# Performance work log

Hardware: AMD Instinct MI355X
Metric: run time of the kernel (lower is better)

Reference implementation:

```python
import jax, jax.numpy as jnp
import numpy as np

D_MODEL = 1024
NHEAD = 16
HEAD_DIM = D_MODEL // NHEAD
B, T = 2, 2048


def setup_inputs() -> dict:
    key = jax.random.key(0)
    ks = jax.random.split(key, 12)
    s = 1.0 / np.sqrt(D_MODEL)
    return {
        "query": jax.random.normal(ks[0], (B, T, D_MODEL), jnp.float32),
        "key": jax.random.normal(ks[1], (B, T, D_MODEL), jnp.float32),
        "value": jax.random.normal(ks[2], (B, T, D_MODEL), jnp.float32),
        "key_padding_mask": jnp.zeros((B, T), dtype=bool),
        "attn_mask": jnp.zeros((T, T), jnp.float32),
        "stoich_frac": jax.random.uniform(ks[3], (B, T), jnp.float32),
        "Wq": jax.random.uniform(ks[4], (D_MODEL, D_MODEL), jnp.float32, -s, s),
        "bq": jnp.zeros((D_MODEL,), jnp.float32),
        "Wk": jax.random.uniform(ks[5], (D_MODEL, D_MODEL), jnp.float32, -s, s),
        "bk": jnp.zeros((D_MODEL,), jnp.float32),
        "Wv": jax.random.uniform(ks[6], (D_MODEL, D_MODEL), jnp.float32, -s, s),
        "bv": jnp.zeros((D_MODEL,), jnp.float32),
        "Wo": jax.random.uniform(ks[7], (D_MODEL, D_MODEL), jnp.float32, -s, s),
        "bo": jnp.zeros((D_MODEL,), jnp.float32),
        "stoich_alpha": jnp.float32(0.1),
    }


def reference(query, key, value, key_padding_mask, attn_mask, stoich_frac,
              Wq, bq, Wk, bk, Wv, bv, Wo, bo, stoich_alpha):
    Bq, Tq, _ = query.shape
    Tk = key.shape[1]
    scale = HEAD_DIM ** -0.5
    # Linear projections (torch Linear: x @ W.T + b), reshape to [B, H, T, Dh]
    Q = (query @ Wq.T + bq).reshape(Bq, Tq, NHEAD, HEAD_DIM).transpose(0, 2, 1, 3)
    K = (key @ Wk.T + bk).reshape(Bq, Tk, NHEAD, HEAD_DIM).transpose(0, 2, 1, 3)
    V = (value @ Wv.T + bv).reshape(Bq, Tk, NHEAD, HEAD_DIM).transpose(0, 2, 1, 3)
    # Scores [B, H, Tq, Tk]
    scores = jnp.einsum("bhqd,bhkd->bhqk", Q, K) * scale
    # Stoichiometric pairwise bias (T_q == T_k path)
    diff = stoich_frac[:, :, None] - stoich_frac[:, None, :]  # [B, Tq, Tk]
    bias = stoich_alpha * (jnp.log1p(jnp.abs(diff)) * jnp.sign(diff))
    scores = scores + bias[:, None, :, :]
    scores = scores + attn_mask  # broadcasts [Tq, Tk]
    scores = jnp.where(key_padding_mask[:, None, None, :], -jnp.inf, scores)
    probs = jax.nn.softmax(scores, axis=-1)
    # dropout: eval mode / p=0 -> identity
    out = jnp.einsum("bhqk,bhkd->bhqd", probs, V)
    out = out.transpose(0, 2, 1, 3).reshape(Bq, Tq, D_MODEL)
    return out @ Wo.T + bo
```

## Files before the change

### kernel.cpp

```cpp
#include <hip/hip_runtime.h>
#include <math.h>

typedef __bf16 bf16_t;
typedef __bf16 bf16x8 __attribute__((ext_vector_type(8)));
typedef __bf16 bf16x4 __attribute__((ext_vector_type(4)));
typedef float  f32x4  __attribute__((ext_vector_type(4)));

#define NHEAD 16
#define HDIM 64
#define DMODEL 1024
#define TSEQ 2048
#define WEL (DMODEL * DMODEL)

#define SBAR() __builtin_amdgcn_s_barrier()
#define SCHED0() __builtin_amdgcn_sched_barrier(0)
#define LGKM0() do { asm volatile("s_waitcnt lgkmcnt(0)" ::: "memory"); \
                     __builtin_amdgcn_sched_barrier(0); } while (0)

__device__ __forceinline__ f32x4 mfma16(bf16x8 a, bf16x8 b, f32x4 c) {
  return __builtin_amdgcn_mfma_f32_16x16x32_bf16(a, b, c, 0, 0, 0);
}

__device__ __forceinline__ void gload16(const bf16_t* g, bf16_t* l) {
  __builtin_amdgcn_global_load_lds((const __attribute__((address_space(1))) void*)g,
                                   (__attribute__((address_space(3))) void*)l, 16, 0, 0);
}

__device__ __forceinline__ unsigned pk2(float lo, float hi) {
  unsigned short a = __builtin_bit_cast(unsigned short, (__bf16)lo);
  unsigned short c = __builtin_bit_cast(unsigned short, (__bf16)hi);
  return ((unsigned)c << 16) | a;
}

__device__ __forceinline__ void cvtstore(f32x4 x0, f32x4 x1, bf16_t* dh, bf16_t* dl, int off) {
  bf16x8 hfr, lfr;
#pragma unroll
  for (int j = 0; j < 4; ++j) {
    float v = x0[j];
    __bf16 hb = (__bf16)v;
    hfr[j] = hb; lfr[j] = (__bf16)(v - (float)hb);
    float w = x1[j];
    __bf16 wb = (__bf16)w;
    hfr[4 + j] = wb; lfr[4 + j] = (__bf16)(w - (float)wb);
  }
  *(bf16x8*)(dh + off) = hfr;
  *(bf16x8*)(dl + off) = lfr;
}

__global__ __launch_bounds__(256)
void presplit_w(const float* __restrict__ w0, const float* __restrict__ w1,
                const float* __restrict__ w2, const float* __restrict__ w3,
                bf16_t* __restrict__ out) {
  const int y = blockIdx.y;
  const float* src = (y == 0) ? w0 : (y == 1) ? w1 : (y == 2) ? w2 : w3;
  size_t i = ((size_t)blockIdx.x * 256 + threadIdx.x) * 8;
  f32x4 a = *(const f32x4*)(src + i);
  f32x4 c = *(const f32x4*)(src + i + 4);
  bf16x8 h, l;
#pragma unroll
  for (int j = 0; j < 4; ++j) {
    __bf16 hb = (__bf16)a[j];
    h[j] = hb; l[j] = (__bf16)(a[j] - (float)hb);
    __bf16 cb = (__bf16)c[j];
    h[4 + j] = cb; l[4 + j] = (__bf16)(c[j] - (float)cb);
  }
  bf16_t* dh = out + (size_t)y * 2 * WEL;
  *(bf16x8*)(dh + i) = h;
  *(bf16x8*)(dh + WEL + i) = l;
}

__global__ __launch_bounds__(256)
void build_bias(const float* __restrict__ amask, const unsigned char* __restrict__ kpm,
                const float* __restrict__ sf, const float* __restrict__ alpha_p,
                bf16_t* __restrict__ BM) {
  size_t idx = (size_t)blockIdx.x * 256 + threadIdx.x;
  int k8 = (int)(idx & (TSEQ / 8 - 1));
  size_t bq = idx >> 8;
  int b = (int)(bq >> 11);
  int q = (int)(bq & (TSEQ - 1));
  const float sfq = sf[bq];
  const float alpha = *alpha_p;
  const float* sfk = sf + (size_t)b * TSEQ + k8 * 8;
  const float* am  = amask + (size_t)q * TSEQ + k8 * 8;
  const unsigned char* kp = kpm + (size_t)b * TSEQ + k8 * 8;
  bf16x8 o;
#pragma unroll
  for (int j = 0; j < 8; ++j) {
    float df = sfq - sfk[j];
    float v = alpha * copysignf(log1pf(fabsf(df)), df) + am[j];
    if (kp[j]) v = -1.0e30f;
    o[j] = (__bf16)v;
  }
  *(bf16x8*)&BM[idx * 8] = o;
}

template<int MODE>
__global__ __launch_bounds__(512)
void gemm_qkv(const float* __restrict__ A, const bf16_t* __restrict__ Wh,
              const bf16_t* __restrict__ Wl, const float* __restrict__ bias,
              bf16_t* __restrict__ obh, bf16_t* __restrict__ obl) {
  __shared__ bf16_t AH[8 * 512], AL[8 * 512], WHs[2][4 * 512], WLs[2][4 * 512];
  const int tid = threadIdx.x;
  const int lane = tid & 63;
  const int a15 = lane & 15, g = lane >> 4;
  const int wv = tid >> 6, wm = wv >> 1, wn = wv & 1;
  const int m0 = blockIdx.y * 128, n0 = blockIdx.x * 64;
  f32x4 acc[2][2] = {};

  const int t0 = tid >> 6, l0 = tid & 63;
  const float* pA = A + (size_t)(m0 + t0 * 16 + (l0 & 15)) * DMODEL + 8 * (l0 >> 4);
  const int wts = wv & 3;
  const bf16_t* pWg = ((wv < 4) ? Wh : Wl) + (size_t)(n0 + wts * 16 + a15) * DMODEL + 8 * g;

  f32x4 rAa = *(const f32x4*)pA, rAb = *(const f32x4*)(pA + 4);
  gload16(pWg, (wv < 4) ? &WHs[0][wts * 512] : &WLs[0][wts * 512]);

  constexpr int NK = DMODEL / 32;
  for (int t = 0; t < NK; ++t) {
    const int cur = t & 1;
    SBAR();
    cvtstore(rAa, rAb, AH, AL, tid * 8);
    SCHED0();
    if (t + 1 < NK) {
      pA += 32;
      rAa = *(const f32x4*)pA; rAb = *(const f32x4*)(pA + 4);
      SCHED0();
      gload16(pWg + (t + 1) * 32, (wv < 4) ? &WHs[cur ^ 1][wts * 512]
                                           : &WLs[cur ^ 1][wts * 512]);
      SCHED0();
      asm volatile("s_waitcnt vmcnt(3)" ::: "memory");
    } else {
      asm volatile("s_waitcnt vmcnt(0)" ::: "memory");
    }
    LGKM0();
    SBAR();

    bf16x8 ah[2], al[2], wh[2], wl[2];
#pragma unroll
    for (int i = 0; i < 2; ++i) {
      ah[i] = *(const bf16x8*)&AH[(wm * 2 + i) * 512 + lane * 8];
      al[i] = *(const bf16x8*)&AL[(wm * 2 + i) * 512 + lane * 8];
      wh[i] = *(const bf16x8*)&WHs[cur][(wn * 2 + i) * 512 + lane * 8];
      wl[i] = *(const bf16x8*)&WLs[cur][(wn * 2 + i) * 512 + lane * 8];
    }
    __builtin_amdgcn_s_setprio(1);
    if (MODE == 2) {
#pragma unroll
      for (int i = 0; i < 2; ++i)
#pragma unroll
        for (int j = 0; j < 2; ++j) {
          acc[i][j] = mfma16(wh[i], ah[j], acc[i][j]);
          acc[i][j] = mfma16(wh[i], al[j], acc[i][j]);
          acc[i][j] = mfma16(wl[i], ah[j], acc[i][j]);
        }
    } else {
#pragma unroll
      for (int i = 0; i < 2; ++i)
#pragma unroll
        for (int j = 0; j < 2; ++j) {
          acc[i][j] = mfma16(ah[i], wh[j], acc[i][j]);
          acc[i][j] = mfma16(ah[i], wl[j], acc[i][j]);
          acc[i][j] = mfma16(al[i], wh[j], acc[i][j]);
        }
    }
    __builtin_amdgcn_s_setprio(0);
  }

  if (MODE == 1) {
#pragma unroll
    for (int i = 0; i < 2; ++i)
#pragma unroll
      for (int j = 0; j < 2; ++j) {
        int n = n0 + wn * 32 + j * 16 + a15;
        float bs = bias[n];
        int hh = n >> 6, d = n & 63;
#pragma unroll
        for (int r = 0; r < 4; ++r) {
          int m = m0 + wm * 32 + i * 16 + 4 * g + r;
          int bb = m >> 11, t = m & (TSEQ - 1);
          float v = acc[i][j][r] + bs;
          size_t o = (((size_t)(bb * NHEAD + hh)) * TSEQ + t) * HDIM + d;
          __bf16 hb = (__bf16)v;
          obh[o] = hb;
          obl[o] = (__bf16)(v - (float)hb);
        }
      }
  } else {
#pragma unroll
    for (int i = 0; i < 2; ++i)
#pragma unroll
      for (int j = 0; j < 2; ++j) {
        int m = m0 + wm * 32 + j * 16 + a15;
        int bb = m >> 11, t = m & (TSEQ - 1);
#pragma unroll
        for (int r = 0; r < 4; ++r) {
          int n = n0 + wn * 32 + i * 16 + 4 * g + r;
          float v = acc[i][j][r] + bias[n];
          int hh = n >> 6, d = n & 63;
          size_t o = (((size_t)(bb * NHEAD + hh)) * HDIM + d) * TSEQ + t;
          __bf16 hb = (__bf16)v;
          obh[o] = hb;
          obl[o] = (__bf16)(v - (float)hb);
        }
      }
  }
}

__global__ __launch_bounds__(512)
void gemm_out(const bf16_t* __restrict__ Ah, const bf16_t* __restrict__ Al,
              const bf16_t* __restrict__ Wh, const bf16_t* __restrict__ Wl,
              const float* __restrict__ bias, float* __restrict__ of) {
  __shared__ bf16_t AHs[2][8 * 512], ALs[2][8 * 512], WHs[2][4 * 512], WLs[2][4 * 512];
  const int tid = threadIdx.x;
  const int lane = tid & 63;
  const int a15 = lane & 15, g = lane >> 4;
  const int wv = tid >> 6, wm = wv >> 1, wn = wv & 1;
  const int m0 = blockIdx.y * 128, n0 = blockIdx.x * 64;
  f32x4 acc[2][2] = {};

  const bf16_t* pAh = Ah + (size_t)(m0 + wv * 16 + a15) * DMODEL + 8 * g;
  const bf16_t* pAl = Al + (size_t)(m0 + wv * 16 + a15) * DMODEL + 8 * g;
  const int wts = wv & 3;
  const bf16_t* pWg = ((wv < 4) ? Wh : Wl) + (size_t)(n0 + wts * 16 + a15) * DMODEL + 8 * g;

  auto stage = [&](int t, int buf) {
    gload16(pAh + t * 32, &AHs[buf][wv * 512]);
    gload16(pAl + t * 32, &ALs[buf][wv * 512]);
    gload16(pWg + t * 32, (wv < 4) ? &WHs[buf][wts * 512] : &WLs[buf][wts * 512]);
  };
  stage(0, 0);

  constexpr int NK = DMODEL / 32;
  for (int t = 0; t < NK; ++t) {
    const int cur = t & 1;
    if (t + 1 < NK) {
      stage(t + 1, cur ^ 1);
      asm volatile("s_waitcnt vmcnt(3)" ::: "memory");
    } else {
      asm volatile("s_waitcnt vmcnt(0)" ::: "memory");
    }
    SCHED0();
    SBAR();

    bf16x8 ah[2], al[2], wh[2], wl[2];
#pragma unroll
    for (int i = 0; i < 2; ++i) {
      ah[i] = *(const bf16x8*)&AHs[cur][(wm * 2 + i) * 512 + lane * 8];
      al[i] = *(const bf16x8*)&ALs[cur][(wm * 2 + i) * 512 + lane * 8];
      wh[i] = *(const bf16x8*)&WHs[cur][(wn * 2 + i) * 512 + lane * 8];
      wl[i] = *(const bf16x8*)&WLs[cur][(wn * 2 + i) * 512 + lane * 8];
    }
    __builtin_amdgcn_s_setprio(1);
#pragma unroll
    for (int i = 0; i < 2; ++i)
#pragma unroll
      for (int j = 0; j < 2; ++j) {
        acc[i][j] = mfma16(ah[i], wh[j], acc[i][j]);
        acc[i][j] = mfma16(ah[i], wl[j], acc[i][j]);
        acc[i][j] = mfma16(al[i], wh[j], acc[i][j]);
      }
    __builtin_amdgcn_s_setprio(0);
    SBAR();
  }

#pragma unroll
  for (int i = 0; i < 2; ++i)
#pragma unroll
    for (int j = 0; j < 2; ++j) {
      int n = n0 + wn * 32 + j * 16 + a15;
      float bs = bias[n];
#pragma unroll
      for (int r = 0; r < 4; ++r) {
        int m = m0 + wm * 32 + i * 16 + 4 * g + r;
        of[(size_t)m * DMODEL + n] = acc[i][j][r] + bs;
      }
    }
}

__global__ __launch_bounds__(512)
void attn_mfma(const bf16_t* __restrict__ Qhi, const bf16_t* __restrict__ Qlo,
               const bf16_t* __restrict__ Khi, const bf16_t* __restrict__ Klo,
               const bf16_t* __restrict__ Vth, const bf16_t* __restrict__ Vtl,
               const bf16_t* __restrict__ BMt,
               bf16_t* __restrict__ Oh, bf16_t* __restrict__ Ol) {
  __shared__ bf16_t KH[2][8 * 512], KL[2][8 * 512], VH[2][8 * 512], VL[2][8 * 512];
  __shared__ bf16_t PS[8 * 512];
  const int tid = threadIdx.x;
  const int lane = tid & 63, wv = tid >> 6;
  const int a15 = lane & 15, g = lane >> 4;
  const int b = blockIdx.z, h = blockIdx.y, q0 = blockIdx.x * 128;
  const int bh = b * NHEAD + h;
  const int qg = q0 + wv * 16 + a15;
  constexpr int NT = TSEQ / 64;

  const bf16_t* Qh_b = Qhi + ((size_t)bh * TSEQ + qg) * HDIM;
  const bf16_t* Ql_b = Qlo + ((size_t)bh * TSEQ + qg) * HDIM;
  const bf16_t* Kh_b = Khi + (size_t)bh * TSEQ * HDIM;
  const bf16_t* Kl_b = Klo + (size_t)bh * TSEQ * HDIM;
  const bf16_t* Vh_b = Vth + (size_t)bh * HDIM * TSEQ;
  const bf16_t* Vl_b = Vtl + (size_t)bh * HDIM * TSEQ;
  const bf16_t* bmrow = BMt + ((size_t)b * TSEQ + qg) * TSEQ;

  bf16x8 qh[2], ql[2];
  qh[0] = *(const bf16x8*)&Qh_b[8 * g];
  qh[1] = *(const bf16x8*)&Qh_b[32 + 8 * g];
  ql[0] = *(const bf16x8*)&Ql_b[8 * g];
  ql[1] = *(const bf16x8*)&Ql_b[32 + 8 * g];

  f32x4 aco[4] = {};
  float m_run = -3.0e38f, l_run = 0.f;
  bf16x4 bmv[4], bmn[4];

  const int ts = wv >> 1, ks = wv & 1;
  auto stage = [&](int k0, int buf) {
    size_t ko = (size_t)(k0 + 16 * ts + a15) * HDIM + 32 * ks + 8 * g;
    gload16(Kh_b + ko, &KH[buf][wv * 512]);
    gload16(Kl_b + ko, &KL[buf][wv * 512]);
    size_t vo = (size_t)(16 * ts + a15) * TSEQ + k0 + 32 * ks + 8 * g;
    gload16(Vh_b + vo, &VH[buf][wv * 512]);
    gload16(Vl_b + vo, &VL[buf][wv * 512]);
  };

#pragma unroll
  for (int mt = 0; mt < 4; ++mt) bmv[mt] = *(const bf16x4*)&bmrow[16 * mt + 4 * g];
  stage(0, 0);

  const int psb = wv * 512 + a15 * 32;
  const int r3 = a15 & 3;

  for (int t = 0; t < NT; ++t) {
    const int cur = t & 1;
    if (t + 1 < NT) {
      const int kn = (t + 1) * 64;
#pragma unroll
      for (int mt = 0; mt < 4; ++mt) bmn[mt] = *(const bf16x4*)&bmrow[kn + 16 * mt + 4 * g];
      stage(kn, cur ^ 1);
      asm volatile("s_waitcnt vmcnt(8)" ::: "memory");
    } else {
      asm volatile("s_waitcnt vmcnt(0)" ::: "memory");
    }
    SCHED0();
    SBAR();

    f32x4 s4[4];
    __builtin_amdgcn_s_setprio(1);
#pragma unroll
    for (int mt = 0; mt < 4; ++mt) {
      bf16x8 k0h = *(const bf16x8*)&KH[cur][(mt * 2 + 0) * 512 + lane * 8];
      bf16x8 k1h = *(const bf16x8*)&KH[cur][(mt * 2 + 1) * 512 + lane * 8];
      bf16x8 k0l = *(const bf16x8*)&KL[cur][(mt * 2 + 0) * 512 + lane * 8];
      bf16x8 k1l = *(const bf16x8*)&KL[cur][(mt * 2 + 1) * 512 + lane * 8];
      f32x4 sa = {};
      sa = mfma16(k0h, qh[0], sa);
      sa = mfma16(k1h, qh[1], sa);
      sa = mfma16(k0h, ql[0], sa);
      sa = mfma16(k1h, ql[1], sa);
      sa = mfma16(k0l, qh[0], sa);
      sa = mfma16(k1l, qh[1], sa);
      s4[mt] = sa;
    }
    __builtin_amdgcn_s_setprio(0);

#pragma unroll
    for (int mt = 0; mt < 4; ++mt)
#pragma unroll
      for (int r = 0; r < 4; ++r)
        s4[mt][r] = fmaf(s4[mt][r], 0.125f, (float)bmv[mt][r]);

    float tmax = -3.0e38f;
#pragma unroll
    for (int mt = 0; mt < 4; ++mt)
#pragma unroll
      for (int r = 0; r < 4; ++r) tmax = fmaxf(tmax, s4[mt][r]);
    tmax = fmaxf(tmax, __shfl_xor(tmax, 16));
    tmax = fmaxf(tmax, __shfl_xor(tmax, 32));
    if (!__all(tmax - m_run <= 8.0f)) {
      float mnew = fmaxf(m_run, tmax);
      float corr = __expf(m_run - mnew);
      l_run *= corr;
#pragma unroll
      for (int dt = 0; dt < 4; ++dt) aco[dt] *= corr;
      m_run = mnew;
    }
    float psum = 0.f;
    unsigned pk01[4], pk23[4];
#pragma unroll
    for (int mt = 0; mt < 4; ++mt) {
      float p0 = __expf(s4[mt][0] - m_run);
      float p1 = __expf(s4[mt][1] - m_run);
      float p2 = __expf(s4[mt][2] - m_run);
      float p3 = __expf(s4[mt][3] - m_run);
      psum += (p0 + p1) + (p2 + p3);
      pk01[mt] = pk2(p0, p1);
      pk23[mt] = pk2(p2, p3);
    }
    psum += __shfl_xor(psum, 16);
    psum += __shfl_xor(psum, 32);
    l_run += psum;

    __builtin_amdgcn_s_setprio(1);
#pragma unroll
    for (int kss = 0; kss < 2; ++kss) {
#pragma unroll
      for (int mh = 0; mh < 2; ++mh) {
        int mt = kss * 2 + mh;
        int phys = ((mh << 1) | (g >> 1)) ^ r3;
        uint2 w2;
        w2.x = pk01[mt];
        w2.y = pk23[mt];
        *(uint2*)&PS[psb + phys * 8 + (g & 1) * 4] = w2;
      }
      LGKM0();
      bf16x8 pf = *(const bf16x8*)&PS[psb + ((g ^ r3) << 3)];
#pragma unroll
      for (int dt = 0; dt < 4; ++dt) {
        bf16x8 vh = *(const bf16x8*)&VH[cur][(dt * 2 + kss) * 512 + lane * 8];
        bf16x8 vl = *(const bf16x8*)&VL[cur][(dt * 2 + kss) * 512 + lane * 8];
        aco[dt] = mfma16(vh, pf, aco[dt]);
        aco[dt] = mfma16(vl, pf, aco[dt]);
      }
    }
    __builtin_amdgcn_s_setprio(0);

    if (t + 1 < NT) {
#pragma unroll
      for (int mt = 0; mt < 4; ++mt) bmv[mt] = bmn[mt];
    }
    SBAR();
  }

  float inv = 1.0f / l_run;
#pragma unroll
  for (int dt = 0; dt < 4; ++dt) {
    f32x4 o = aco[dt] * inv;
    bf16x4 oh, ol;
#pragma unroll
    for (int r = 0; r < 4; ++r) {
      __bf16 hb = (__bf16)o[r];
      oh[r] = hb;
      ol[r] = (__bf16)(o[r] - (float)hb);
    }
    size_t off = ((size_t)b * TSEQ + qg) * DMODEL + h * HDIM + dt * 16 + 4 * g;
    *(bf16x4*)&Oh[off] = oh;
    *(bf16x4*)&Ol[off] = ol;
  }
}

extern "C" void kernel_launch(void* const* d_in, const int* in_sizes, int n_in,
                              void* d_out, int out_size, void* d_ws, size_t ws_size,
                              hipStream_t stream) {
  const float* query = (const float*)d_in[0];
  const float* key = (const float*)d_in[1];
  const float* value = (const float*)d_in[2];
  const unsigned char* kpm = (const unsigned char*)d_in[3];
  const float* amask = (const float*)d_in[4];
  const float* sf = (const float*)d_in[5];
  const float* Wq = (const float*)d_in[6];
  const float* bq = (const float*)d_in[7];
  const float* Wk = (const float*)d_in[8];
  const float* bk = (const float*)d_in[9];
  const float* Wv = (const float*)d_in[10];
  const float* bv = (const float*)d_in[11];
  const float* Wo = (const float*)d_in[12];
  const float* bo = (const float*)d_in[13];
  const float* alpha = (const float*)d_in[14];
  float* out = (float*)d_out;

  const size_t NEL = (size_t)2 * NHEAD * TSEQ * HDIM;
  bf16_t* p = (bf16_t*)d_ws;
  bf16_t* Qh = p;
  bf16_t* Ql = p + NEL;
  bf16_t* Kh = p + 2 * NEL;
  bf16_t* Kl = p + 3 * NEL;
  bf16_t* Vh = p + 4 * NEL;
  bf16_t* Vl = p + 5 * NEL;
  bf16_t* Oh = p + 6 * NEL;
  bf16_t* Ol = p + 7 * NEL;
  bf16_t* BMt = p + 8 * NEL;
  bf16_t* wsp = p + 10 * NEL;
  bf16_t* wqh = wsp + 0 * WEL, *wql = wsp + 1 * WEL;
  bf16_t* wkh = wsp + 2 * WEL, *wkl = wsp + 3 * WEL;
  bf16_t* wvh = wsp + 4 * WEL, *wvl = wsp + 5 * WEL;
  bf16_t* woh = wsp + 6 * WEL, *wol = wsp + 7 * WEL;

  presplit_w<<<dim3(WEL / (256 * 8), 4), dim3(256), 0, stream>>>(Wq, Wk, Wv, Wo, wsp);
  build_bias<<<dim3(4096), dim3(256), 0, stream>>>(amask, kpm, sf, alpha, BMt);

  dim3 gg(16, 32), gb(512);
  gemm_qkv<1><<<gg, gb, 0, stream>>>(query, wqh, wql, bq, Qh, Ql);
  gemm_qkv<1><<<gg, gb, 0, stream>>>(key, wkh, wkl, bk, Kh, Kl);
  gemm_qkv<2><<<gg, gb, 0, stream>>>(value, wvh, wvl, bv, Vh, Vl);
  dim3 ga(TSEQ / 128, NHEAD, 2);
  attn_mfma<<<ga, gb, 0, stream>>>(Qh, Ql, Kh, Kl, Vh, Vl, BMt, Oh, Ol);
  gemm_out<<<gg, gb, 0, stream>>>(Oh, Ol, woh, wol, bo, out);
}
```

Before: 347.2 us.

## Enlarge GEMM M tile to 256 and load weights straight into registers

The projection and output GEMMs now cover 256 rows per block instead of 128, so each warp computes a 64x32 tile. Weight fragments are loaded from global memory directly into registers with one-step register prefetch, no longer staged through shared memory. In the QKV GEMM the A tile is double-buffered in LDS, which removes one barrier per k-step. This halves the grid (256 blocks) and raises register pressure, which may lower occupancy or under-fill the CUs, in exchange for more reuse of the weight tiles.

```diff
diff --git a/kernel.cpp b/kernel.cpp
--- a/kernel.cpp
+++ b/kernel.cpp
@@ -99,76 +99,95 @@
 void gemm_qkv(const float* __restrict__ A, const bf16_t* __restrict__ Wh,
               const bf16_t* __restrict__ Wl, const float* __restrict__ bias,
               bf16_t* __restrict__ obh, bf16_t* __restrict__ obl) {
-  __shared__ bf16_t AH[8 * 512], AL[8 * 512], WHs[2][4 * 512], WLs[2][4 * 512];
+  __shared__ bf16_t AH[2][16 * 512], AL[2][16 * 512];
   const int tid = threadIdx.x;
   const int lane = tid & 63;
   const int a15 = lane & 15, g = lane >> 4;
   const int wv = tid >> 6, wm = wv >> 1, wn = wv & 1;
-  const int m0 = blockIdx.y * 128, n0 = blockIdx.x * 64;
-  f32x4 acc[2][2] = {};
+  const int m0 = blockIdx.y * 256, n0 = blockIdx.x * 64;
+  constexpr int NI = (MODE == 2) ? 2 : 4;
+  constexpr int NJ = (MODE == 2) ? 4 : 2;
+  f32x4 acc[NI][NJ] = {};
 
   const int t0 = tid >> 6, l0 = tid & 63;
-  const float* pA = A + (size_t)(m0 + t0 * 16 + (l0 & 15)) * DMODEL + 8 * (l0 >> 4);
-  const int wts = wv & 3;
-  const bf16_t* pWg = ((wv < 4) ? Wh : Wl) + (size_t)(n0 + wts * 16 + a15) * DMODEL + 8 * g;
-
-  f32x4 rAa = *(const f32x4*)pA, rAb = *(const f32x4*)(pA + 4);
-  gload16(pWg, (wv < 4) ? &WHs[0][wts * 512] : &WLs[0][wts * 512]);
+  const float* pA0 = A + (size_t)(m0 + t0 * 16 + (l0 & 15)) * DMODEL + 8 * (l0 >> 4);
+  const float* pA1 = pA0 + (size_t)128 * DMODEL;
+  const bf16_t* pWh0 = Wh + (size_t)(n0 + wn * 32 + a15) * DMODEL + 8 * g;
+  const bf16_t* pWl0 = Wl + (size_t)(n0 + wn * 32 + a15) * DMODEL + 8 * g;
+
+  f32x4 rA0a = *(const f32x4*)pA0, rA0b = *(const f32x4*)(pA0 + 4);
+  f32x4 rA1a = *(const f32x4*)pA1, rA1b = *(const f32x4*)(pA1 + 4);
+  cvtstore(rA0a, rA0b, AH[0], AL[0], tid * 8);
+  cvtstore(rA1a, rA1b, AH[0], AL[0], (tid + 512) * 8);
+  bf16x8 whc[2], wlc[2], whn[2], wln[2];
+  whc[0] = *(const bf16x8*)(pWh0);
+  whc[1] = *(const bf16x8*)(pWh0 + 16 * DMODEL);
+  wlc[0] = *(const bf16x8*)(pWl0);
+  wlc[1] = *(const bf16x8*)(pWl0 + 16 * DMODEL);
+  pA0 += 32; pA1 += 32;
+  rA0a = *(const f32x4*)pA0; rA0b = *(const f32x4*)(pA0 + 4);
+  rA1a = *(const f32x4*)pA1; rA1b = *(const f32x4*)(pA1 + 4);
+  LGKM0();
+  SBAR();
 
   constexpr int NK = DMODEL / 32;
   for (int t = 0; t < NK; ++t) {
     const int cur = t & 1;
-    SBAR();
-    cvtstore(rAa, rAb, AH, AL, tid * 8);
+    bf16x8 ah[4], al[4];
+#pragma unroll
+    for (int i = 0; i < 4; ++i) {
+      ah[i] = *(const bf16x8*)&AH[cur][(wm * 4 + i) * 512 + lane * 8];
+      al[i] = *(const bf16x8*)&AL[cur][(wm * 4 + i) * 512 + lane * 8];
+    }
+    if (t + 1 < NK) {
+      const int k = (t + 1) * 32;
+      whn[0] = *(const bf16x8*)(pWh0 + k);
+      whn[1] = *(const bf16x8*)(pWh0 + 16 * DMODEL + k);
+      wln[0] = *(const bf16x8*)(pWl0 + k);
+      wln[1] = *(const bf16x8*)(pWl0 + 16 * DMODEL + k);
+    }
+    SCHED0();
+    __builtin_amdgcn_s_setprio(1);
+    if (MODE == 2) {
+#pragma unroll
+      for (int i = 0; i < 2; ++i)
+#pragma unroll
+        for (int j = 0; j < 4; ++j) {
+          acc[i][j] = mfma16(whc[i], ah[j], acc[i][j]);
+          acc[i][j] = mfma16(whc[i], al[j], acc[i][j]);
+          acc[i][j] = mfma16(wlc[i], ah[j], acc[i][j]);
+        }
+    } else {
+#pragma unroll
+      for (int i = 0; i < 4; ++i)
+#pragma unroll
+        for (int j = 0; j < 2; ++j) {
+          acc[i][j] = mfma16(ah[i], whc[j], acc[i][j]);
+          acc[i][j] = mfma16(ah[i], wlc[j], acc[i][j]);
+          acc[i][j] = mfma16(al[i], whc[j], acc[i][j]);
+        }
+    }
+    __builtin_amdgcn_s_setprio(0);
     SCHED0();
     if (t + 1 < NK) {
-      pA += 32;
-      rAa = *(const f32x4*)pA; rAb = *(const f32x4*)(pA + 4);
+      cvtstore(rA0a, rA0b, AH[cur ^ 1], AL[cur ^ 1], tid * 8);
+      cvtstore(rA1a, rA1b, AH[cur ^ 1], AL[cur ^ 1], (tid + 512) * 8);
       SCHED0();
-      gload16(pWg + (t + 1) * 32, (wv < 4) ? &WHs[cur ^ 1][wts * 512]
-                                           : &WLs[cur ^ 1][wts * 512]);
-      SCHED0();
-      asm volatile("s_waitcnt vmcnt(3)" ::: "memory");
-    } else {
-      asm volatile("s_waitcnt vmcnt(0)" ::: "memory");
+      if (t + 2 < NK) {
+        pA0 += 32; pA1 += 32;
+        rA0a = *(const f32x4*)pA0; rA0b = *(const f32x4*)(pA0 + 4);
+        rA1a = *(const f32x4*)pA1; rA1b = *(const f32x4*)(pA1 + 4);
+      }
+      whc[0] = whn[0]; whc[1] = whn[1];
+      wlc[0] = wln[0]; wlc[1] = wln[1];
     }
     LGKM0();
     SBAR();
-
-    bf16x8 ah[2], al[2], wh[2], wl[2];
-#pragma unroll
-    for (int i = 0; i < 2; ++i) {
-      ah[i] = *(const bf16x8*)&AH[(wm * 2 + i) * 512 + lane * 8];
-      al[i] = *(const bf16x8*)&AL[(wm * 2 + i) * 512 + lane * 8];
-      wh[i] = *(const bf16x8*)&WHs[cur][(wn * 2 + i) * 512 + lane * 8];
-      wl[i] = *(const bf16x8*)&WLs[cur][(wn * 2 + i) * 512 + lane * 8];
-    }
-    __builtin_amdgcn_s_setprio(1);
-    if (MODE == 2) {
-#pragma unroll
-      for (int i = 0; i < 2; ++i)
-#pragma unroll
-        for (int j = 0; j < 2; ++j) {
-          acc[i][j] = mfma16(wh[i], ah[j], acc[i][j]);
-          acc[i][j] = mfma16(wh[i], al[j], acc[i][j]);
-          acc[i][j] = mfma16(wl[i], ah[j], acc[i][j]);
-        }
-    } else {
-#pragma unroll
-      for (int i = 0; i < 2; ++i)
-#pragma unroll
-        for (int j = 0; j < 2; ++j) {
-          acc[i][j] = mfma16(ah[i], wh[j], acc[i][j]);
-          acc[i][j] = mfma16(ah[i], wl[j], acc[i][j]);
-          acc[i][j] = mfma16(al[i], wh[j], acc[i][j]);
-        }
-    }
-    __builtin_amdgcn_s_setprio(0);
   }
 
   if (MODE == 1) {
 #pragma unroll
-    for (int i = 0; i < 2; ++i)
+    for (int i = 0; i < 4; ++i)
 #pragma unroll
       for (int j = 0; j < 2; ++j) {
         int n = n0 + wn * 32 + j * 16 + a15;
@@ -176,7 +195,7 @@
         int hh = n >> 6, d = n & 63;
 #pragma unroll
         for (int r = 0; r < 4; ++r) {
-          int m = m0 + wm * 32 + i * 16 + 4 * g + r;
+          int m = m0 + wm * 64 + i * 16 + 4 * g + r;
           int bb = m >> 11, t = m & (TSEQ - 1);
           float v = acc[i][j][r] + bs;
           size_t o = (((size_t)(bb * NHEAD + hh)) * TSEQ + t) * HDIM + d;
@@ -189,8 +208,8 @@
 #pragma unroll
     for (int i = 0; i < 2; ++i)
 #pragma unroll
-      for (int j = 0; j < 2; ++j) {
-        int m = m0 + wm * 32 + j * 16 + a15;
+      for (int j = 0; j < 4; ++j) {
+        int m = m0 + wm * 64 + j * 16 + a15;
         int bb = m >> 11, t = m & (TSEQ - 1);
 #pragma unroll
         for (int r = 0; r < 4; ++r) {
@@ -210,68 +229,84 @@
 void gemm_out(const bf16_t* __restrict__ Ah, const bf16_t* __restrict__ Al,
               const bf16_t* __restrict__ Wh, const bf16_t* __restrict__ Wl,
               const float* __restrict__ bias, float* __restrict__ of) {
-  __shared__ bf16_t AHs[2][8 * 512], ALs[2][8 * 512], WHs[2][4 * 512], WLs[2][4 * 512];
+  __shared__ bf16_t AHs[2][16 * 512], ALs[2][16 * 512];
   const int tid = threadIdx.x;
   const int lane = tid & 63;
   const int a15 = lane & 15, g = lane >> 4;
   const int wv = tid >> 6, wm = wv >> 1, wn = wv & 1;
-  const int m0 = blockIdx.y * 128, n0 = blockIdx.x * 64;
-  f32x4 acc[2][2] = {};
-
-  const bf16_t* pAh = Ah + (size_t)(m0 + wv * 16 + a15) * DMODEL + 8 * g;
-  const bf16_t* pAl = Al + (size_t)(m0 + wv * 16 + a15) * DMODEL + 8 * g;
-  const int wts = wv & 3;
-  const bf16_t* pWg = ((wv < 4) ? Wh : Wl) + (size_t)(n0 + wts * 16 + a15) * DMODEL + 8 * g;
-
-  auto stage = [&](int t, int buf) {
-    gload16(pAh + t * 32, &AHs[buf][wv * 512]);
-    gload16(pAl + t * 32, &ALs[buf][wv * 512]);
-    gload16(pWg + t * 32, (wv < 4) ? &WHs[buf][wts * 512] : &WLs[buf][wts * 512]);
+  const int m0 = blockIdx.y * 256, n0 = blockIdx.x * 64;
+  f32x4 acc[4][2] = {};
+
+  const bf16_t* pAh0 = Ah + (size_t)(m0 + (2 * wv) * 16 + a15) * DMODEL + 8 * g;
+  const bf16_t* pAh1 = Ah + (size_t)(m0 + (2 * wv + 1) * 16 + a15) * DMODEL + 8 * g;
+  const bf16_t* pAl0 = Al + (size_t)(m0 + (2 * wv) * 16 + a15) * DMODEL + 8 * g;
+  const bf16_t* pAl1 = Al + (size_t)(m0 + (2 * wv + 1) * 16 + a15) * DMODEL + 8 * g;
+  const bf16_t* pWh0 = Wh + (size_t)(n0 + wn * 32 + a15) * DMODEL + 8 * g;
+  const bf16_t* pWl0 = Wl + (size_t)(n0 + wn * 32 + a15) * DMODEL + 8 * g;
+
+  auto stageA = [&](int t, int buf) {
+    gload16(pAh0 + t * 32, &AHs[buf][(2 * wv) * 512]);
+    gload16(pAh1 + t * 32, &AHs[buf][(2 * wv + 1) * 512]);
+    gload16(pAl0 + t * 32, &ALs[buf][(2 * wv) * 512]);
+    gload16(pAl1 + t * 32, &ALs[buf][(2 * wv + 1) * 512]);
   };
-  stage(0, 0);
+
+  bf16x8 whc[2], wlc[2], whn[2], wln[2];
+  stageA(0, 0);
+  whc[0] = *(const bf16x8*)(pWh0);
+  whc[1] = *(const bf16x8*)(pWh0 + 16 * DMODEL);
+  wlc[0] = *(const bf16x8*)(pWl0);
+  wlc[1] = *(const bf16x8*)(pWl0 + 16 * DMODEL);
 
   constexpr int NK = DMODEL / 32;
   for (int t = 0; t < NK; ++t) {
     const int cur = t & 1;
     if (t + 1 < NK) {
-      stage(t + 1, cur ^ 1);
-      asm volatile("s_waitcnt vmcnt(3)" ::: "memory");
+      const int k = (t + 1) * 32;
+      stageA(t + 1, cur ^ 1);
+      whn[0] = *(const bf16x8*)(pWh0 + k);
+      whn[1] = *(const bf16x8*)(pWh0 + 16 * DMODEL + k);
+      wln[0] = *(const bf16x8*)(pWl0 + k);
+      wln[1] = *(const bf16x8*)(pWl0 + 16 * DMODEL + k);
+      asm volatile("s_waitcnt vmcnt(8)" ::: "memory");
     } else {
       asm volatile("s_waitcnt vmcnt(0)" ::: "memory");
     }
     SCHED0();
     SBAR();
 
-    bf16x8 ah[2], al[2], wh[2], wl[2];
-#pragma unroll
-    for (int i = 0; i < 2; ++i) {
-      ah[i] = *(const bf16x8*)&AHs[cur][(wm * 2 + i) * 512 + lane * 8];
-      al[i] = *(const bf16x8*)&ALs[cur][(wm * 2 + i) * 512 + lane * 8];
-      wh[i] = *(const bf16x8*)&WHs[cur][(wn * 2 + i) * 512 + lane * 8];
-      wl[i] = *(const bf16x8*)&WLs[cur][(wn * 2 + i) * 512 + lane * 8];
+    bf16x8 ah[4], al[4];
+#pragma unroll
+    for (int i = 0; i < 4; ++i) {
+      ah[i] = *(const bf16x8*)&AHs[cur][(wm * 4 + i) * 512 + lane * 8];
+      al[i] = *(const bf16x8*)&ALs[cur][(wm * 4 + i) * 512 + lane * 8];
     }
     __builtin_amdgcn_s_setprio(1);
 #pragma unroll
-    for (int i = 0; i < 2; ++i)
+    for (int i = 0; i < 4; ++i)
 #pragma unroll
       for (int j = 0; j < 2; ++j) {
-        acc[i][j] = mfma16(ah[i], wh[j], acc[i][j]);
-        acc[i][j] = mfma16(ah[i], wl[j], acc[i][j]);
-        acc[i][j] = mfma16(al[i], wh[j], acc[i][j]);
+        acc[i][j] = mfma16(ah[i], whc[j], acc[i][j]);
+        acc[i][j] = mfma16(ah[i], wlc[j], acc[i][j]);
+        acc[i][j] = mfma16(al[i], whc[j], acc[i][j]);
       }
     __builtin_amdgcn_s_setprio(0);
+    if (t + 1 < NK) {
+      whc[0] = whn[0]; whc[1] = whn[1];
+      wlc[0] = wln[0]; wlc[1] = wln[1];
+    }
     SBAR();
   }
 
 #pragma unroll
-  for (int i = 0; i < 2; ++i)
+  for (int i = 0; i < 4; ++i)
 #pragma unroll
     for (int j = 0; j < 2; ++j) {
       int n = n0 + wn * 32 + j * 16 + a15;
       float bs = bias[n];
 #pragma unroll
       for (int r = 0; r < 4; ++r) {
-        int m = m0 + wm * 32 + i * 16 + 4 * g + r;
+        int m = m0 + wm * 64 + i * 16 + 4 * g + r;
         of[(size_t)m * DMODEL + n] = acc[i][j][r] + bs;
       }
     }
@@ -486,7 +521,7 @@
   presplit_w<<<dim3(WEL / (256 * 8), 4), dim3(256), 0, stream>>>(Wq, Wk, Wv, Wo, wsp);
   build_bias<<<dim3(4096), dim3(256), 0, stream>>>(amask, kpm, sf, alpha, BMt);
 
-  dim3 gg(16, 32), gb(512);
+  dim3 gg(DMODEL / 64, 4096 / 256), gb(512);
   gemm_qkv<1><<<gg, gb, 0, stream>>>(query, wqh, wql, bq, Qh, Ql);
   gemm_qkv<1><<<gg, gb, 0, stream>>>(key, wkh, wkl, bk, Kh, Kl);
   gemm_qkv<2><<<gg, gb, 0, stream>>>(value, wvh, wvl, bv, Vh, Vl);
```

After: 418.1 us. 20.4% more time.

## Fuse Q/K/V projection GEMMs into one launch and defer softmax row-sum reduction

Applied to the files above, without the earlier changes.

The three separate QKV projection GEMM launches become a single launch with a z-dimension of 3, choosing inputs, weights, bias and outputs per blockIdx.z and turning the template mode into a runtime branch. This removes two kernel launches and lets all three projections share the GPU at once, giving better occupancy across 1536 blocks. Separately, the attention kernel now accumulates per-lane partial row sums and does the cross-lane shuffle reduction once after the loop instead of every iteration. That is valid because the correction factor is uniform across the reduced lanes. The runtime vmode branch may cost a little in register allocation or code quality.

```diff
diff --git a/kernel.cpp b/kernel.cpp
--- a/kernel.cpp
+++ b/kernel.cpp
@@ -94,12 +94,22 @@
   *(bf16x8*)&BM[idx * 8] = o;
 }
 
-template<int MODE>
 __global__ __launch_bounds__(512)
-void gemm_qkv(const float* __restrict__ A, const bf16_t* __restrict__ Wh,
-              const bf16_t* __restrict__ Wl, const float* __restrict__ bias,
-              bf16_t* __restrict__ obh, bf16_t* __restrict__ obl) {
+void gemm_qkv_fused(const float* __restrict__ Aq, const float* __restrict__ Ak,
+                    const float* __restrict__ Av, const bf16_t* __restrict__ wsp,
+                    const float* __restrict__ bq, const float* __restrict__ bk,
+                    const float* __restrict__ bv, bf16_t* __restrict__ outbase) {
   __shared__ bf16_t AH[8 * 512], AL[8 * 512], WHs[2][4 * 512], WLs[2][4 * 512];
+  const int z = blockIdx.z;
+  const float* A = (z == 0) ? Aq : (z == 1) ? Ak : Av;
+  const bf16_t* Wh = wsp + (size_t)2 * z * WEL;
+  const bf16_t* Wl = Wh + WEL;
+  const float* bias = (z == 0) ? bq : (z == 1) ? bk : bv;
+  const size_t NELq = (size_t)2 * NHEAD * TSEQ * HDIM;
+  bf16_t* obh = outbase + (size_t)2 * z * NELq;
+  bf16_t* obl = obh + NELq;
+  const bool vmode = (z == 2);
+
   const int tid = threadIdx.x;
   const int lane = tid & 63;
   const int a15 = lane & 15, g = lane >> 4;
@@ -144,7 +154,7 @@
       wl[i] = *(const bf16x8*)&WLs[cur][(wn * 2 + i) * 512 + lane * 8];
     }
     __builtin_amdgcn_s_setprio(1);
-    if (MODE == 2) {
+    if (vmode) {
 #pragma unroll
       for (int i = 0; i < 2; ++i)
 #pragma unroll
@@ -166,7 +176,7 @@
     __builtin_amdgcn_s_setprio(0);
   }
 
-  if (MODE == 1) {
+  if (!vmode) {
 #pragma unroll
     for (int i = 0; i < 2; ++i)
 #pragma unroll
@@ -394,8 +404,6 @@
       pk01[mt] = pk2(p0, p1);
       pk23[mt] = pk2(p2, p3);
     }
-    psum += __shfl_xor(psum, 16);
-    psum += __shfl_xor(psum, 32);
     l_run += psum;
 
     __builtin_amdgcn_s_setprio(1);
@@ -428,6 +436,9 @@
     }
     SBAR();
   }
+
+  l_run += __shfl_xor(l_run, 16);
+  l_run += __shfl_xor(l_run, 32);
 
   float inv = 1.0f / l_run;
 #pragma unroll
@@ -478,19 +489,18 @@
   bf16_t* Ol = p + 7 * NEL;
   bf16_t* BMt = p + 8 * NEL;
   bf16_t* wsp = p + 10 * NEL;
-  bf16_t* wqh = wsp + 0 * WEL, *wql = wsp + 1 * WEL;
-  bf16_t* wkh = wsp + 2 * WEL, *wkl = wsp + 3 * WEL;
-  bf16_t* wvh = wsp + 4 * WEL, *wvl = wsp + 5 * WEL;
   bf16_t* woh = wsp + 6 * WEL, *wol = wsp + 7 * WEL;
 
   presplit_w<<<dim3(WEL / (256 * 8), 4), dim3(256), 0, stream>>>(Wq, Wk, Wv, Wo, wsp);
   build_bias<<<dim3(4096), dim3(256), 0, stream>>>(amask, kpm, sf, alpha, BMt);
 
-  dim3 gg(16, 32), gb(512);
-  gemm_qkv<1><<<gg, gb, 0, stream>>>(query, wqh, wql, bq, Qh, Ql);
-  gemm_qkv<1><<<gg, gb, 0, stream>>>(key, wkh, wkl, bk, Kh, Kl);
-  gemm_qkv<2><<<gg, gb, 0, stream>>>(value, wvh, wvl, bv, Vh, Vl);
+  dim3 gb(512);
+  dim3 gq(16, 32, 3);
+  gemm_qkv_fused<<<gq, gb, 0, stream>>>(query, key, value, wsp, bq, bk, bv, p);
+
   dim3 ga(TSEQ / 128, NHEAD, 2);
   attn_mfma<<<ga, gb, 0, stream>>>(Qh, Ql, Kh, Kl, Vh, Vl, BMt, Oh, Ol);
+
+  dim3 gg(16, 32);
   gemm_out<<<gg, gb, 0, stream>>>(Oh, Ol, woh, wol, bo, out);
 }
```

Measured after the change: 340.3 us. -2.0%, faster.

## Presplit activations to bf16 hi/lo and unify GEMMs with async LDS loads

Applied to the files above, without the earlier changes.

Adds a presplit_a kernel that converts query, key and value from fp32 into bf16 hi/lo pairs once, so the QKV GEMMs can stream their A operand straight into LDS with global_load_lds. This removes the in-loop register load, conversion and LDS store, and lets all four GEMMs share a single double-buffered template. It also moves the cross-lane softmax row-sum shuffle out of the attention inner loop to a single reduction at the end. The cost is an extra kernel launch and a round trip of the split activations through global memory, and the workspace layout grows to hold them.

```diff
diff --git a/kernel.cpp b/kernel.cpp
--- a/kernel.cpp
+++ b/kernel.cpp
@@ -30,21 +30,6 @@
   unsigned short a = __builtin_bit_cast(unsigned short, (__bf16)lo);
   unsigned short c = __builtin_bit_cast(unsigned short, (__bf16)hi);
   return ((unsigned)c << 16) | a;
-}
-
-__device__ __forceinline__ void cvtstore(f32x4 x0, f32x4 x1, bf16_t* dh, bf16_t* dl, int off) {
-  bf16x8 hfr, lfr;
-#pragma unroll
-  for (int j = 0; j < 4; ++j) {
-    float v = x0[j];
-    __bf16 hb = (__bf16)v;
-    hfr[j] = hb; lfr[j] = (__bf16)(v - (float)hb);
-    float w = x1[j];
-    __bf16 wb = (__bf16)w;
-    hfr[4 + j] = wb; lfr[4 + j] = (__bf16)(w - (float)wb);
-  }
-  *(bf16x8*)(dh + off) = hfr;
-  *(bf16x8*)(dl + off) = lfr;
 }
 
 __global__ __launch_bounds__(256)
@@ -67,6 +52,27 @@
   bf16_t* dh = out + (size_t)y * 2 * WEL;
   *(bf16x8*)(dh + i) = h;
   *(bf16x8*)(dh + WEL + i) = l;
+}
+
+__global__ __launch_bounds__(256)
+void presplit_a(const float* __restrict__ a0, const float* __restrict__ a1,
+                const float* __restrict__ a2, bf16_t* __restrict__ out, size_t nel) {
+  const int y = blockIdx.y;
+  const float* src = (y == 0) ? a0 : (y == 1) ? a1 : a2;
+  size_t i = ((size_t)blockIdx.x * 256 + threadIdx.x) * 8;
+  f32x4 a = *(const f32x4*)(src + i);
+  f32x4 c = *(const f32x4*)(src + i + 4);
+  bf16x8 h, l;
+#pragma unroll
+  for (int j = 0; j < 4; ++j) {
+    __bf16 hb = (__bf16)a[j];
+    h[j] = hb; l[j] = (__bf16)(a[j] - (float)hb);
+    __bf16 cb = (__bf16)c[j];
+    h[4 + j] = cb; l[4 + j] = (__bf16)(c[j] - (float)cb);
+  }
+  bf16_t* dh = out + (size_t)y * 2 * nel;
+  *(bf16x8*)(dh + i) = h;
+  *(bf16x8*)(dh + nel + i) = l;
 }
 
 __global__ __launch_bounds__(256)
@@ -96,10 +102,12 @@
 
 template<int MODE>
 __global__ __launch_bounds__(512)
-void gemm_qkv(const float* __restrict__ A, const bf16_t* __restrict__ Wh,
-              const bf16_t* __restrict__ Wl, const float* __restrict__ bias,
-              bf16_t* __restrict__ obh, bf16_t* __restrict__ obl) {
-  __shared__ bf16_t AH[8 * 512], AL[8 * 512], WHs[2][4 * 512], WLs[2][4 * 512];
+void gemm_bf16(const bf16_t* __restrict__ Ah, const bf16_t* __restrict__ Al,
+               const bf16_t* __restrict__ Wh, const bf16_t* __restrict__ Wl,
+               const float* __restrict__ bias,
+               bf16_t* __restrict__ obh, bf16_t* __restrict__ obl,
+               float* __restrict__ of) {
+  __shared__ bf16_t AHs[2][8 * 512], ALs[2][8 * 512], WHs[2][4 * 512], WLs[2][4 * 512];
   const int tid = threadIdx.x;
   const int lane = tid & 63;
   const int a15 = lane & 15, g = lane >> 4;
@@ -107,44 +115,40 @@
   const int m0 = blockIdx.y * 128, n0 = blockIdx.x * 64;
   f32x4 acc[2][2] = {};
 
-  const int t0 = tid >> 6, l0 = tid & 63;
-  const float* pA = A + (size_t)(m0 + t0 * 16 + (l0 & 15)) * DMODEL + 8 * (l0 >> 4);
+  const bf16_t* pAh = Ah + (size_t)(m0 + wv * 16 + a15) * DMODEL + 8 * g;
+  const bf16_t* pAl = Al + (size_t)(m0 + wv * 16 + a15) * DMODEL + 8 * g;
   const int wts = wv & 3;
   const bf16_t* pWg = ((wv < 4) ? Wh : Wl) + (size_t)(n0 + wts * 16 + a15) * DMODEL + 8 * g;
 
-  f32x4 rAa = *(const f32x4*)pA, rAb = *(const f32x4*)(pA + 4);
-  gload16(pWg, (wv < 4) ? &WHs[0][wts * 512] : &WLs[0][wts * 512]);
+  auto stage = [&](int t, int buf) {
+    gload16(pAh + t * 32, &AHs[buf][wv * 512]);
+    gload16(pAl + t * 32, &ALs[buf][wv * 512]);
+    gload16(pWg + t * 32, (wv < 4) ? &WHs[buf][wts * 512] : &WLs[buf][wts * 512]);
+  };
+  stage(0, 0);
 
   constexpr int NK = DMODEL / 32;
   for (int t = 0; t < NK; ++t) {
     const int cur = t & 1;
-    SBAR();
-    cvtstore(rAa, rAb, AH, AL, tid * 8);
-    SCHED0();
     if (t + 1 < NK) {
-      pA += 32;
-      rAa = *(const f32x4*)pA; rAb = *(const f32x4*)(pA + 4);
-      SCHED0();
-      gload16(pWg + (t + 1) * 32, (wv < 4) ? &WHs[cur ^ 1][wts * 512]
-                                           : &WLs[cur ^ 1][wts * 512]);
-      SCHED0();
+      stage(t + 1, cur ^ 1);
       asm volatile("s_waitcnt vmcnt(3)" ::: "memory");
     } else {
       asm volatile("s_waitcnt vmcnt(0)" ::: "memory");
     }
-    LGKM0();
+    SCHED0();
     SBAR();
 
     bf16x8 ah[2], al[2], wh[2], wl[2];
 #pragma unroll
     for (int i = 0; i < 2; ++i) {
-      ah[i] = *(const bf16x8*)&AH[(wm * 2 + i) * 512 + lane * 8];
-      al[i] = *(const bf16x8*)&AL[(wm * 2 + i) * 512 + lane * 8];
+      ah[i] = *(const bf16x8*)&AHs[cur][(wm * 2 + i) * 512 + lane * 8];
+      al[i] = *(const bf16x8*)&ALs[cur][(wm * 2 + i) * 512 + lane * 8];
       wh[i] = *(const bf16x8*)&WHs[cur][(wn * 2 + i) * 512 + lane * 8];
       wl[i] = *(const bf16x8*)&WLs[cur][(wn * 2 + i) * 512 + lane * 8];
     }
     __builtin_amdgcn_s_setprio(1);
-    if (MODE == 2) {
+    if constexpr (MODE == 2) {
 #pragma unroll
       for (int i = 0; i < 2; ++i)
 #pragma unroll
@@ -164,9 +168,23 @@
         }
     }
     __builtin_amdgcn_s_setprio(0);
-  }
-
-  if (MODE == 1) {
+    SBAR();
+  }
+
+  if constexpr (MODE == 0) {
+#pragma unroll
+    for (int i = 0; i < 2; ++i)
+#pragma unroll
+      for (int j = 0; j < 2; ++j) {
+        int n = n0 + wn * 32 + j * 16 + a15;
+        float bs = bias[n];
+#pragma unroll
+        for (int r = 0; r < 4; ++r) {
+          int m = m0 + wm * 32 + i * 16 + 4 * g + r;
+          of[(size_t)m * DMODEL + n] = acc[i][j][r] + bs;
+        }
+      }
+  } else if constexpr (MODE == 1) {
 #pragma unroll
     for (int i = 0; i < 2; ++i)
 #pragma unroll
@@ -204,77 +222,6 @@
         }
       }
   }
-}
-
-__global__ __launch_bounds__(512)
-void gemm_out(const bf16_t* __restrict__ Ah, const bf16_t* __restrict__ Al,
-              const bf16_t* __restrict__ Wh, const bf16_t* __restrict__ Wl,
-              const float* __restrict__ bias, float* __restrict__ of) {
-  __shared__ bf16_t AHs[2][8 * 512], ALs[2][8 * 512], WHs[2][4 * 512], WLs[2][4 * 512];
-  const int tid = threadIdx.x;
-  const int lane = tid & 63;
-  const int a15 = lane & 15, g = lane >> 4;
-  const int wv = tid >> 6, wm = wv >> 1, wn = wv & 1;
-  const int m0 = blockIdx.y * 128, n0 = blockIdx.x * 64;
-  f32x4 acc[2][2] = {};
-
-  const bf16_t* pAh = Ah + (size_t)(m0 + wv * 16 + a15) * DMODEL + 8 * g;
-  const bf16_t* pAl = Al + (size_t)(m0 + wv * 16 + a15) * DMODEL + 8 * g;
-  const int wts = wv & 3;
-  const bf16_t* pWg = ((wv < 4) ? Wh : Wl) + (size_t)(n0 + wts * 16 + a15) * DMODEL + 8 * g;
-
-  auto stage = [&](int t, int buf) {
-    gload16(pAh + t * 32, &AHs[buf][wv * 512]);
-    gload16(pAl + t * 32, &ALs[buf][wv * 512]);
-    gload16(pWg + t * 32, (wv < 4) ? &WHs[buf][wts * 512] : &WLs[buf][wts * 512]);
-  };
-  stage(0, 0);
-
-  constexpr int NK = DMODEL / 32;
-  for (int t = 0; t < NK; ++t) {
-    const int cur = t & 1;
-    if (t + 1 < NK) {
-      stage(t + 1, cur ^ 1);
-      asm volatile("s_waitcnt vmcnt(3)" ::: "memory");
-    } else {
-      asm volatile("s_waitcnt vmcnt(0)" ::: "memory");
-    }
-    SCHED0();
-    SBAR();
-
-    bf16x8 ah[2], al[2], wh[2], wl[2];
-#pragma unroll
-    for (int i = 0; i < 2; ++i) {
-      ah[i] = *(const bf16x8*)&AHs[cur][(wm * 2 + i) * 512 + lane * 8];
-      al[i] = *(const bf16x8*)&ALs[cur][(wm * 2 + i) * 512 + lane * 8];
-      wh[i] = *(const bf16x8*)&WHs[cur][(wn * 2 + i) * 512 + lane * 8];
-      wl[i] = *(const bf16x8*)&WLs[cur][(wn * 2 + i) * 512 + lane * 8];
-    }
-    __builtin_amdgcn_s_setprio(1);
-#pragma unroll
-    for (int i = 0; i < 2; ++i)
-#pragma unroll
-      for (int j = 0; j < 2; ++j) {
-        acc[i][j] = mfma16(ah[i], wh[j], acc[i][j]);
-        acc[i][j] = mfma16(ah[i], wl[j], acc[i][j]);
-        acc[i][j] = mfma16(al[i], wh[j], acc[i][j]);
-      }
-    __builtin_amdgcn_s_setprio(0);
-    SBAR();
-  }
-
-#pragma unroll
-  for (int i = 0; i < 2; ++i)
-#pragma unroll
-    for (int j = 0; j < 2; ++j) {
-      int n = n0 + wn * 32 + j * 16 + a15;
-      float bs = bias[n];
-#pragma unroll
-      for (int r = 0; r < 4; ++r) {
-        int m = m0 + wm * 32 + i * 16 + 4 * g + r;
-        of[(size_t)m * DMODEL + n] = acc[i][j][r] + bs;
-      }
-    }
 }
 
 __global__ __launch_bounds__(512)
@@ -394,8 +341,6 @@
       pk01[mt] = pk2(p0, p1);
       pk23[mt] = pk2(p2, p3);
     }
-    psum += __shfl_xor(psum, 16);
-    psum += __shfl_xor(psum, 32);
     l_run += psum;
 
     __builtin_amdgcn_s_setprio(1);
@@ -428,6 +373,9 @@
     }
     SBAR();
   }
+
+  l_run += __shfl_xor(l_run, 16);
+  l_run += __shfl_xor(l_run, 32);
 
   float inv = 1.0f / l_run;
 #pragma unroll
@@ -468,29 +416,33 @@
 
   const size_t NEL = (size_t)2 * NHEAD * TSEQ * HDIM;
   bf16_t* p = (bf16_t*)d_ws;
-  bf16_t* Qh = p;
-  bf16_t* Ql = p + NEL;
-  bf16_t* Kh = p + 2 * NEL;
-  bf16_t* Kl = p + 3 * NEL;
-  bf16_t* Vh = p + 4 * NEL;
-  bf16_t* Vl = p + 5 * NEL;
-  bf16_t* Oh = p + 6 * NEL;
-  bf16_t* Ol = p + 7 * NEL;
-  bf16_t* BMt = p + 8 * NEL;
-  bf16_t* wsp = p + 10 * NEL;
+  bf16_t* acts = p;
+  bf16_t* Oh = p;
+  bf16_t* Ol = p + NEL;
+  bf16_t* Qh = p + 6 * NEL;
+  bf16_t* Ql = p + 7 * NEL;
+  bf16_t* Kh = p + 8 * NEL;
+  bf16_t* Kl = p + 9 * NEL;
+  bf16_t* Vh = p + 10 * NEL;
+  bf16_t* Vl = p + 11 * NEL;
+  bf16_t* BMt = p + 12 * NEL;
+  bf16_t* wsp = p + 14 * NEL;
   bf16_t* wqh = wsp + 0 * WEL, *wql = wsp + 1 * WEL;
   bf16_t* wkh = wsp + 2 * WEL, *wkl = wsp + 3 * WEL;
   bf16_t* wvh = wsp + 4 * WEL, *wvl = wsp + 5 * WEL;
   bf16_t* woh = wsp + 6 * WEL, *wol = wsp + 7 * WEL;
 
   presplit_w<<<dim3(WEL / (256 * 8), 4), dim3(256), 0, stream>>>(Wq, Wk, Wv, Wo, wsp);
+  presplit_a<<<dim3(NEL / (256 * 8), 3), dim3(256), 0, stream>>>(query, key, value, acts, NEL);
   build_bias<<<dim3(4096), dim3(256), 0, stream>>>(amask, kpm, sf, alpha, BMt);
 
   dim3 gg(16, 32), gb(512);
-  gemm_qkv<1><<<gg, gb, 0, stream>>>(query, wqh, wql, bq, Qh, Ql);
-  gemm_qkv<1><<<gg, gb, 0, stream>>>(key, wkh, wkl, bk, Kh, Kl);
-  gemm_qkv<2><<<gg, gb, 0, stream>>>(value, wvh, wvl, bv, Vh, Vl);
+  gemm_bf16<1><<<gg, gb, 0, stream>>>(acts, acts + NEL, wqh, wql, bq, Qh, Ql, nullptr);
+  gemm_bf16<1><<<gg, gb, 0, stream>>>(acts + 2 * NEL, acts + 3 * NEL, wkh, wkl, bk, Kh, Kl, nullptr);
+  gemm_bf16<2><<<gg, gb, 0, stream>>>(acts + 4 * NEL, acts + 5 * NEL, wvh, wvl, bv, Vh, Vl, nullptr);
+
   dim3 ga(TSEQ / 128, NHEAD, 2);
   attn_mfma<<<ga, gb, 0, stream>>>(Qh, Ql, Kh, Kl, Vh, Vl, BMt, Oh, Ol);
-  gemm_out<<<gg, gb, 0, stream>>>(Oh, Ol, woh, wol, bo, out);
-}
+
+  gemm_bf16<0><<<gg, gb, 0, stream>>>(Oh, Ol, woh, wol, bo, nullptr, nullptr, out);
+}
```

Result: slower. 364.8 us (+5.1%).
